# Kernel optimization log

Hardware: AMD Instinct MI355X
Metric: run time of the kernel (lower is better)

## Reference

```python
import jax, jax.numpy as jnp
import numpy as np
import math

B, IMG, P, C_IN = 32, 32, 2, 4
D, TED, L, H = 768, 256, 12, 12
GRID = IMG // P            # 16
N = GRID * GRID            # 256 patches
HD = D // H                # 64 head dim
MLP_H = 4 * D
RPD = 2 * GRID - 1         # 31 relative-position table side


def _ln(x, w, b, eps=1e-6):
    m = x.mean(-1, keepdims=True)
    v = ((x - m) ** 2).mean(-1, keepdims=True)
    return (x - m) * jax.lax.rsqrt(v + eps) * w + b


def _rel_idx():
    c = jnp.arange(GRID)
    ch, cw = jnp.meshgrid(c, c, indexing='ij')
    cf = jnp.stack([ch.reshape(-1), cw.reshape(-1)])          # [2, N]
    rel = cf[:, :, None] - cf[:, None, :] + (GRID - 1)        # [2, N, N] in [0, 2*GRID-2]
    return rel[0], rel[1]


def setup_inputs() -> dict:
    key = jax.random.key(0)
    ks = iter(jax.random.split(key, 64))
    def nrm(shape, s=0.02):
        return jax.random.normal(next(ks), shape, jnp.float32) * s
    z = lambda *s: jnp.zeros(s, jnp.float32)
    o = lambda *s: jnp.ones(s, jnp.float32)
    return dict(
        x=jax.random.normal(next(ks), (B, C_IN, IMG, IMG), jnp.float32),
        t=jax.random.uniform(next(ks), (B,), jnp.float32) * 1000.0,
        patch_w=nrm((D, C_IN, P, P), 0.5), patch_b=z(D),
        pos_embed=nrm((1, N, D)),
        t_w1=nrm((TED, D)), t_b1=z(D), t_w2=nrm((D, D)), t_b2=z(D),
        norm1_w=o(L, D), norm1_b=z(L, D),
        wqs=nrm((L, D, D)), bqs=z(L, D), wqt=nrm((L, D, D)), bqt=z(L, D),
        wks=nrm((L, D, D)), bks=z(L, D), wkt=nrm((L, D, D)), bkt=z(L, D),
        wvs=nrm((L, D, D)), bvs=z(L, D), wvt=nrm((L, D, D)), bvt=z(L, D),
        attn_proj_w=nrm((L, D, D)), attn_proj_b=z(L, D),
        rpb=nrm((L, RPD, RPD, H)),
        norm2_w=o(L, D), norm2_b=z(L, D),
        mlp_w1=nrm((L, D, MLP_H)), mlp_b1=z(L, MLP_H),
        mlp_w2=nrm((L, MLP_H, D)), mlp_b2=z(L, D),
        norm_w=o(D), norm_b=z(D),
        dec_w=nrm((D, P * P * C_IN)), dec_b=z(P * P * C_IN),
    )


def reference(x, t, patch_w, patch_b, pos_embed, t_w1, t_b1, t_w2, t_b2,
              norm1_w, norm1_b, wqs, bqs, wqt, bqt, wks, bks, wkt, bkt,
              wvs, bvs, wvt, bvt, attn_proj_w, attn_proj_b, rpb,
              norm2_w, norm2_b, mlp_w1, mlp_b1, mlp_w2, mlp_b2,
              norm_w, norm_b, dec_w, dec_b):
    Bn = x.shape[0]
    # patch embed: stride==kernel Conv2d as reshape + einsum -> [B, N, D]
    xr = x.reshape(Bn, C_IN, GRID, P, GRID, P)
    x_s = jnp.einsum('bcipjq,ecpq->bije', xr, patch_w).reshape(Bn, N, D) + patch_b
    x_s = x_s + pos_embed
    # sinusoidal time embedding + MLP -> [B, D]
    half = TED // 2
    freq = jnp.exp(jnp.arange(half, dtype=jnp.float32) * (-math.log(10000.0) / (half - 1)))
    emb = t[:, None] * freq[None, :]
    emb = jnp.concatenate([jnp.sin(emb), jnp.cos(emb)], axis=-1)
    x_t = jax.nn.silu(emb @ t_w1 + t_b1) @ t_w2 + t_b2
    ih, iw = _rel_idx()
    scale = HD ** -0.5
    for l in range(L):
        h = _ln(x_s, norm1_w[l], norm1_b[l])
        q = h @ wqs[l] + bqs[l] + (x_t @ wqt[l] + bqt[l])[:, None, :]
        k = h @ wks[l] + bks[l] + (x_t @ wkt[l] + bkt[l])[:, None, :]
        v = h @ wvs[l] + bvs[l] + (x_t @ wvt[l] + bvt[l])[:, None, :]
        q = q.reshape(Bn, N, H, HD)
        k = k.reshape(Bn, N, H, HD)
        v = v.reshape(Bn, N, H, HD)
        bias = rpb[l][ih, iw]                                  # gather: [N, N, H]
        attn = jnp.einsum('bnhd,bmhd->bhnm', q, k) * scale + bias.transpose(2, 0, 1)[None]
        attn = jax.nn.softmax(attn, axis=-1)
        o_ = jnp.einsum('bhnm,bmhd->bnhd', attn, v).reshape(Bn, N, D)
        x_s = x_s + (o_ @ attn_proj_w[l] + attn_proj_b[l])
        h2 = _ln(x_s, norm2_w[l], norm2_b[l])
        x_s = x_s + (jax.nn.silu(h2 @ mlp_w1[l] + mlp_b1[l]) @ mlp_w2[l] + mlp_b2[l])
    x_s = _ln(x_s, norm_w, norm_b)
    x_s = x_s @ dec_w + dec_b                                  # [B, N, P*P*C]
    # unpatchify -> [B, C, IMG, IMG]
    xo = x_s.reshape(Bn, GRID, GRID, C_IN, P, P).transpose(0, 3, 1, 4, 2, 5)
    return xo.reshape(Bn, C_IN, GRID * P, GRID * P)
```

## Files before the change

### kernel.cpp

```cpp
#include <hip/hip_runtime.h>
#include <hip/hip_bf16.h>

typedef __attribute__((ext_vector_type(8))) short short8;
typedef __attribute__((ext_vector_type(4))) short s16x4;
typedef __attribute__((ext_vector_type(4))) float f32x4;
typedef __hip_bfloat16 bf16;

#define AS1 __attribute__((address_space(1)))
#define AS3 __attribute__((address_space(3)))

__device__ __forceinline__ float b2f(short u) {
  union { unsigned int i; float f; } x;
  x.i = ((unsigned int)(unsigned short)u) << 16;
  return x.f;
}
__device__ __forceinline__ short f2bs(float f) {
  bf16 t = __float2bfloat16(f);
  return *reinterpret_cast<short*>(&t);
}

__device__ __forceinline__ void gld_lds16(const void* g, void* lds) {
  __builtin_amdgcn_global_load_lds((const AS1 unsigned int*)g,
                                   (AS3 unsigned int*)lds, 16, 0, 0);
}

__global__ void transpose_conv(const float* __restrict__ src, bf16* __restrict__ dst,
                               int R, int C, int row_off, long long layer_stride) {
  __shared__ float t[32][33];
  int l = blockIdx.z;
  int r0 = blockIdx.y * 32;
  int c0 = blockIdx.x * 32;
  int tx = threadIdx.x & 31, ty = threadIdx.x >> 5;
  const float* s = src + (size_t)l * R * C;
#pragma unroll
  for (int i = 0; i < 4; ++i)
    t[ty + i * 8][tx] = s[(size_t)(r0 + ty + i * 8) * C + c0 + tx];
  __syncthreads();
  bf16* d = dst + (size_t)l * layer_stride;
#pragma unroll
  for (int i = 0; i < 4; ++i) {
    int n = c0 + ty + i * 8, k = r0 + tx;
    d[(size_t)(row_off + n) * R + k] = __float2bfloat16(t[tx][ty + i * 8]);
  }
}

__global__ void dec_transpose(const float* __restrict__ dw, bf16* __restrict__ dwT) {
  int idx = blockIdx.x * 256 + threadIdx.x;
  if (idx >= 12288) return;
  int k = idx % 768, j = idx / 768;
  dwT[j * 768 + k] = __float2bfloat16(dw[k * 16 + j]);
}

__global__ void patch_embed(const float* __restrict__ x, const float* __restrict__ pw,
                            const float* __restrict__ pb, const float* __restrict__ pos,
                            float* __restrict__ xs) {
  int idx = blockIdx.x * 256 + threadIdx.x;
  int d = idx % 768;
  int n = (idx / 768) & 255;
  int b = idx / (768 * 256);
  int gi = n >> 4, gj = n & 15;
  float acc = pb[d];
#pragma unroll
  for (int c = 0; c < 4; ++c)
#pragma unroll
    for (int p = 0; p < 2; ++p)
#pragma unroll
      for (int q = 0; q < 2; ++q)
        acc += x[((b * 4 + c) * 32 + gi * 2 + p) * 32 + gj * 2 + q] *
               pw[((d * 4 + c) * 2 + p) * 2 + q];
  xs[idx] = acc + pos[n * 768 + d];
}

__global__ void temb_kernel(const float* __restrict__ t, float* __restrict__ emb) {
  int b = blockIdx.x;
  int i = threadIdx.x;
  float f = __expf((float)i * (-logf(10000.f) / 127.f));
  float e = t[b] * f;
  emb[b * 256 + i] = sinf(e);
  emb[b * 256 + 128 + i] = cosf(e);
}

template <int MODE>
__global__ void smallmm_red(const float* __restrict__ in, const float* __restrict__ w,
                            const float* __restrict__ bias, void* __restrict__ out, int K) {
  int tid = threadIdx.x;
  int s = tid & 7, o = blockIdx.x * 32 + (tid >> 3);
  int d = o % 768, b = o / 768;
  int Ks = K >> 3, k0 = s * Ks;
  const float* ir = in + b * K + k0;
  const float* wr = w + (size_t)k0 * 768 + d;
  float a = 0.f;
  for (int i = 0; i < Ks; ++i) a += ir[i] * wr[(size_t)i * 768];
  a += __shfl_xor(a, 1);
  a += __shfl_xor(a, 2);
  a += __shfl_xor(a, 4);
  if (s == 0) {
    a += bias[d];
    if (MODE == 0) {
      a = a / (1.f + __expf(-a));
      ((float*)out)[o] = a;
    } else {
      ((bf16*)out)[o] = __float2bfloat16(a);
    }
  }
}

__global__ void build_btab_frag(const float* __restrict__ rpb, bf16* __restrict__ btf) {
  int idx = blockIdx.x * 256 + threadIdx.x;
  int t = idx & 65535;
  int lh = idx >> 16;
  int h = lh % 12, l = lh / 12;
  int r = t & 3; t >>= 2;
  int lane = t & 63; t >>= 6;
  int i = t & 3; t >>= 2;
  int w = t & 3; t >>= 2;
  int jb = t & 1; t >>= 1;
  int hc = t & 7;
  int q = w * 64 + i * 16 + (lane & 15);
  int k = hc * 32 + jb * 16 + (lane >> 4) * 4 + r;
  int ih = (q >> 4) - (k >> 4) + 15;
  int iw = (q & 15) - (k & 15) + 15;
  btf[idx] = __float2bfloat16(8.0f * rpb[((l * 31 + ih) * 31 + iw) * 12 + h]);
}

__global__ __launch_bounds__(256) void ln_bf16_kernel(const float* __restrict__ x,
                                                      const float* __restrict__ w,
                                                      const float* __restrict__ b,
                                                      bf16* __restrict__ out) {
  int row = blockIdx.x * 4 + (threadIdx.x >> 6);
  int lane = threadIdx.x & 63;
  const float* xr = x + (size_t)row * 768;
  float v[12];
  float s = 0.f, s2 = 0.f;
#pragma unroll
  for (int k = 0; k < 12; ++k) {
    v[k] = xr[lane + k * 64];
    s += v[k];
    s2 += v[k] * v[k];
  }
#pragma unroll
  for (int off = 32; off; off >>= 1) {
    s += __shfl_xor(s, off);
    s2 += __shfl_xor(s2, off);
  }
  float m = s * (1.f / 768.f);
  float var = s2 * (1.f / 768.f) - m * m;
  float r = rsqrtf(var + 1e-6f);
  bf16* orow = out + (size_t)row * 768;
#pragma unroll
  for (int k = 0; k < 12; ++k) {
    int c = lane + k * 64;
    orow[c] = __float2bfloat16((v[k] - m) * r * w[c] + b[c]);
  }
}

template <int EPI>
__global__ __launch_bounds__(256) void gemm128(
    const bf16* __restrict__ A, int lda, const bf16* __restrict__ BT, int ldb, int K,
    const float* __restrict__ p0, const float* __restrict__ p1,
    const float* __restrict__ p2, const float* __restrict__ p3,
    const float* __restrict__ p4, const float* __restrict__ p5,
    const float* __restrict__ resid, float* __restrict__ outF,
    bf16* __restrict__ outB, int ldc) {
  __shared__ __align__(16) char lds[65536];
  const int tid = threadIdx.x;
  const int wid = tid >> 6, lane = tid & 63;
  const int wr = wid >> 1, wc = wid & 1;
  const int nwg = gridDim.x * gridDim.y;
  const int bid = blockIdx.y * gridDim.x + blockIdx.x;
  const int swzb = (bid & 7) * (nwg >> 3) + (bid >> 3);
  const int m0 = (swzb / gridDim.x) * 128, n0 = (swzb % gridDim.x) * 128;
  const int l16 = lane & 15, lq = lane >> 4;

  f32x4 acc[4][4];
#pragma unroll
  for (int i = 0; i < 4; ++i)
#pragma unroll
    for (int j = 0; j < 4; ++j) acc[i][j] = f32x4{0.f, 0.f, 0.f, 0.f};

  const int arow = tid >> 3;
  const int aslot = (tid & 7) ^ (arow & 7);
  const bf16* gA = A + (size_t)(m0 + arow) * lda + aslot * 8;
  const bf16* gB = BT + (size_t)(n0 + arow) * ldb + aslot * 8;
  const unsigned offw = (unsigned)__builtin_amdgcn_readfirstlane((tid & ~63) * 16);

  const int NT = K >> 6;
  auto stage = [&](int buf, int t) {
    char* p = lds + buf * 32768;
    const int k = t * 64;
#pragma unroll
    for (int it = 0; it < 4; ++it) {
      gld_lds16(gA + (size_t)it * 32 * lda + k, p + it * 4096 + offw);
      gld_lds16(gB + (size_t)it * 32 * ldb + k, p + 16384 + it * 4096 + offw);
    }
  };

  stage(0, 0);
  const unsigned swb = ((unsigned)(l16 & 7)) << 4;
  for (int t = 0; t < NT; ++t) {
    char* cur = lds + (t & 1) * 32768;
    if (t + 1 < NT) {
      stage((t + 1) & 1, t + 1);
      asm volatile("s_waitcnt vmcnt(8)" ::: "memory");
    } else {
      asm volatile("s_waitcnt vmcnt(0)" ::: "memory");
    }
    __builtin_amdgcn_s_barrier();
#pragma unroll
    for (int ks = 0; ks < 2; ++ks) {
      short8 af[4], bfr[4];
      const unsigned ko = ((unsigned)(ks * 64 + lq * 16)) ^ swb;
#pragma unroll
      for (int i = 0; i < 4; ++i) {
        af[i]  = *(const short8*)(cur + (wr * 64 + i * 16 + l16) * 128 + ko);
        bfr[i] = *(const short8*)(cur + 16384 + (wc * 64 + i * 16 + l16) * 128 + ko);
      }
#pragma unroll
      for (int i = 0; i < 4; ++i)
#pragma unroll
        for (int j = 0; j < 4; ++j)
          acc[i][j] = __builtin_amdgcn_mfma_f32_16x16x32_bf16(af[i], bfr[j], acc[i][j], 0, 0, 0);
    }
    __builtin_amdgcn_s_barrier();
  }

#pragma unroll
  for (int i = 0; i < 4; ++i) {
#pragma unroll
    for (int j = 0; j < 4; ++j) {
#pragma unroll
      for (int r = 0; r < 4; ++r) {
        int row = m0 + wr * 64 + i * 16 + lq * 4 + r;
        int col = n0 + wc * 64 + j * 16 + l16;
        float v = acc[i][j][r];
        if constexpr (EPI == 0) {
          int s = col / 768, d = col % 768;
          int b = row >> 8;
          const float* bs = (s == 0) ? p0 : (s == 1) ? p1 : p2;
          const float* ts = (s == 0) ? p3 : (s == 1) ? p4 : p5;
          v += bs[d] + ts[b * 768 + d];
          outB[(size_t)row * ldc + col] = __float2bfloat16(v);
        } else if constexpr (EPI == 1) {
          v += p0[col] + resid[(size_t)row * ldc + col];
          outF[(size_t)row * ldc + col] = v;
        } else if constexpr (EPI == 2) {
          v += p0[col];
          v = v / (1.f + __expf(-v));
          outB[(size_t)row * ldc + col] = __float2bfloat16(v);
        } else if constexpr (EPI == 3) {
          if (row < 32) {
            int l = col / 2304;
            int r2c = col - l * 2304;
            int s = r2c / 768, d = r2c - s * 768;
            const float* bs = (s == 0) ? p0 : (s == 1) ? p1 : p2;
            v += bs[l * 768 + d];
            outF[(size_t)((l * 3 + s) * 32 + row) * 768 + d] = v;
          }
        } else {
          if (col < 16) {
            v += p0[col];
            int b = row >> 8, n = row & 255;
            int gi = n >> 4, gj = n & 15;
            int c = col >> 2, pp = (col >> 1) & 1, qq = col & 1;
            outF[((b * 4 + c) * 32 + gi * 2 + pp) * 32 + gj * 2 + qq] = v;
          }
        }
      }
    }
  }
}

__global__ __launch_bounds__(256) void attn_mfma(const bf16* __restrict__ qkv,
                                                 const bf16* __restrict__ btf,
                                                 bf16* __restrict__ obuf) {
  __shared__ __align__(16) char lds[65536];
  const int tid = threadIdx.x;
  const int wave = tid >> 6, lane = tid & 63;
  const int l16 = lane & 15, lq = lane >> 4;
  const int b = blockIdx.x / 12, h = blockIdx.x % 12;
  const bf16* qb = qkv + (size_t)b * 256 * 2304;

  {
    const short8* vrow = (const short8*)(qb + (size_t)tid * 2304 + 1536 + h * 64);
    short8 vv[8];
#pragma unroll
    for (int c = 0; c < 8; ++c) vv[c] = vrow[c];
#pragma unroll
    for (int c = 0; c < 8; ++c)
#pragma unroll
      for (int e = 0; e < 8; ++e) {
        int d = c * 8 + e;
        unsigned off = (unsigned)(d * 512 + tid * 2) ^ ((unsigned)(d & 7) << 4);
        *(short*)(lds + off) = vv[c][e];
      }
  }
  short8 qf[4][2];
#pragma unroll
  for (int i = 0; i < 4; ++i)
#pragma unroll
    for (int ks = 0; ks < 2; ++ks)
      qf[i][ks] = *(const short8*)(qb + (size_t)(wave * 64 + i * 16 + l16) * 2304 +
                                   h * 64 + ks * 32 + lq * 8);
  __syncthreads();

  f32x4 oacc[4][4];
#pragma unroll
  for (int i = 0; i < 4; ++i)
#pragma unroll
    for (int j = 0; j < 4; ++j) oacc[i][j] = f32x4{0.f, 0.f, 0.f, 0.f};
  float lp[4] = {0.f, 0.f, 0.f, 0.f};
  const bf16* bl = btf + (size_t)h * 65536 + lane * 4;
  const unsigned swzv = ((unsigned)(l16 & 7)) << 4;
  const unsigned swzp = ((unsigned)(l16 & 3)) << 4;

  for (int hc = 0; hc < 8; ++hc) {
    short8 kf[2][2];
#pragma unroll
    for (int jb = 0; jb < 2; ++jb) {
      const bf16* kr = qb + (size_t)(hc * 32 + jb * 16 + l16) * 2304 + 768 + h * 64 + lq * 8;
      kf[jb][0] = *(const short8*)(kr);
      kf[jb][1] = *(const short8*)(kr + 32);
    }
    f32x4 sacc[4][2];
#pragma unroll
    for (int i = 0; i < 4; ++i)
#pragma unroll
      for (int jb = 0; jb < 2; ++jb) {
        s16x4 bv = *(const s16x4*)(bl + ((size_t)((hc * 2 + jb) * 16 + wave * 4 + i) << 8));
        sacc[i][jb] = f32x4{b2f(bv[0]), b2f(bv[1]), b2f(bv[2]), b2f(bv[3])};
      }
#pragma unroll
    for (int jb = 0; jb < 2; ++jb)
#pragma unroll
      for (int i = 0; i < 4; ++i) {
        sacc[i][jb] = __builtin_amdgcn_mfma_f32_16x16x32_bf16(kf[jb][0], qf[i][0], sacc[i][jb], 0, 0, 0);
        sacc[i][jb] = __builtin_amdgcn_mfma_f32_16x16x32_bf16(kf[jb][1], qf[i][1], sacc[i][jb], 0, 0, 0);
      }
    char* Pw = lds + 32768 + (hc & 1) * 16384 + wave * 4096;
#pragma unroll
    for (int i = 0; i < 4; ++i)
#pragma unroll
      for (int jb = 0; jb < 2; ++jb) {
        float p0 = __expf(sacc[i][jb][0] * 0.125f);
        float p1 = __expf(sacc[i][jb][1] * 0.125f);
        float p2 = __expf(sacc[i][jb][2] * 0.125f);
        float p3 = __expf(sacc[i][jb][3] * 0.125f);
        lp[i] += (p0 + p1) + (p2 + p3);
        s16x4 pk = {f2bs(p0), f2bs(p1), f2bs(p2), f2bs(p3)};
        *(s16x4*)(Pw + (i * 16 + l16) * 64 + (((unsigned)(jb * 32 + lq * 8)) ^ swzp)) = pk;
      }
    asm volatile("s_waitcnt lgkmcnt(0)" ::: "memory");
    __builtin_amdgcn_sched_barrier(0);
    short8 pa[4], vb[4];
#pragma unroll
    for (int i = 0; i < 4; ++i)
      pa[i] = *(const short8*)(Pw + (i * 16 + l16) * 64 + (((unsigned)(lq * 16)) ^ swzp));
#pragma unroll
    for (int dj = 0; dj < 4; ++dj)
      vb[dj] = *(const short8*)(lds + (dj * 16 + l16) * 512 +
                                (((unsigned)(hc * 64 + lq * 16)) ^ swzv));
#pragma unroll
    for (int i = 0; i < 4; ++i)
#pragma unroll
      for (int dj = 0; dj < 4; ++dj)
        oacc[i][dj] = __builtin_amdgcn_mfma_f32_16x16x32_bf16(pa[i], vb[dj], oacc[i][dj], 0, 0, 0);
  }

#pragma unroll
  for (int i = 0; i < 4; ++i) {
    float l = lp[i];
    l += __shfl_xor(l, 16);
    l += __shfl_xor(l, 32);
#pragma unroll
    for (int r = 0; r < 4; ++r) {
      float linv = 1.f / __shfl(l, lq * 4 + r);
      int grow = b * 256 + wave * 64 + i * 16 + lq * 4 + r;
#pragma unroll
      for (int dj = 0; dj < 4; ++dj)
        obuf[(size_t)grow * 768 + h * 64 + dj * 16 + l16] =
            __float2bfloat16(oacc[i][dj][r] * linv);
    }
  }
}

extern "C" void kernel_launch(void* const* d_in, const int* in_sizes, int n_in,
                              void* d_out, int out_size, void* d_ws, size_t ws_size,
                              hipStream_t stream) {
  (void)in_sizes; (void)n_in; (void)out_size; (void)ws_size;
  const float* x       = (const float*)d_in[0];
  const float* t_in    = (const float*)d_in[1];
  const float* patch_w = (const float*)d_in[2];
  const float* patch_b = (const float*)d_in[3];
  const float* pos     = (const float*)d_in[4];
  const float* t_w1    = (const float*)d_in[5];
  const float* t_b1    = (const float*)d_in[6];
  const float* t_w2    = (const float*)d_in[7];
  const float* t_b2    = (const float*)d_in[8];
  const float* norm1_w = (const float*)d_in[9];
  const float* norm1_b = (const float*)d_in[10];
  const float* wqs     = (const float*)d_in[11];
  const float* bqs     = (const float*)d_in[12];
  const float* wqt     = (const float*)d_in[13];
  const float* bqt     = (const float*)d_in[14];
  const float* wks     = (const float*)d_in[15];
  const float* bks     = (const float*)d_in[16];
  const float* wkt     = (const float*)d_in[17];
  const float* bkt     = (const float*)d_in[18];
  const float* wvs     = (const float*)d_in[19];
  const float* bvs     = (const float*)d_in[20];
  const float* wvt     = (const float*)d_in[21];
  const float* bvt     = (const float*)d_in[22];
  const float* projw   = (const float*)d_in[23];
  const float* projb   = (const float*)d_in[24];
  const float* rpb     = (const float*)d_in[25];
  const float* norm2_w = (const float*)d_in[26];
  const float* norm2_b = (const float*)d_in[27];
  const float* mlp_w1  = (const float*)d_in[28];
  const float* mlp_b1  = (const float*)d_in[29];
  const float* mlp_w2  = (const float*)d_in[30];
  const float* mlp_b2  = (const float*)d_in[31];
  const float* norm_w  = (const float*)d_in[32];
  const float* norm_b  = (const float*)d_in[33];
  const float* dec_w   = (const float*)d_in[34];
  const float* dec_b   = (const float*)d_in[35];

  char* ws = (char*)d_ws;
  size_t off = 0;
  auto alloc = [&](size_t bytes) -> void* {
    void* p = ws + off;
    off += (bytes + 255) & ~(size_t)255;
    return p;
  };
  bf16* wqkvT = (bf16*)alloc(12ull * 2304 * 768 * 2);
  bf16* projT = (bf16*)alloc(12ull * 768 * 768 * 2);
  bf16* mlp1T = (bf16*)alloc(12ull * 3072 * 768 * 2);
  bf16* mlp2T = (bf16*)alloc(12ull * 768 * 3072 * 2);
  bf16* wtT   = (bf16*)alloc(12ull * 2304 * 768 * 2);
  float* xs   = (float*)alloc(8192ull * 768 * 4);
  bf16* hbuf  = (bf16*)alloc(8192ull * 768 * 2);
  bf16* qkvb  = (bf16*)alloc(8192ull * 2304 * 2);
  bf16* obuf  = (bf16*)alloc(8192ull * 768 * 2);
  bf16* btabf = (bf16*)alloc(12ull * 12 * 256 * 256 * 2);
  float* ttok = (float*)alloc(12ull * 3 * 32 * 768 * 4);
  bf16* xtb   = (bf16*)alloc(128ull * 768 * 2);
  bf16* dwT   = (bf16*)alloc(128ull * 768 * 2);
  float* emb  = (float*)alloc(32ull * 256 * 4);
  float* h1   = (float*)alloc(32ull * 768 * 4);
  bf16* hmlp  = qkvb;

  hipMemsetAsync(xtb, 0, 128ull * 768 * 2, stream);
  hipMemsetAsync(dwT, 0, 128ull * 768 * 2, stream);

  transpose_conv<<<dim3(24, 24, 12), 256, 0, stream>>>(wqs, wqkvT, 768, 768, 0, 2304ll * 768);
  transpose_conv<<<dim3(24, 24, 12), 256, 0, stream>>>(wks, wqkvT, 768, 768, 768, 2304ll * 768);
  transpose_conv<<<dim3(24, 24, 12), 256, 0, stream>>>(wvs, wqkvT, 768, 768, 1536, 2304ll * 768);
  transpose_conv<<<dim3(24, 24, 12), 256, 0, stream>>>(projw, projT, 768, 768, 0, 768ll * 768);
  transpose_conv<<<dim3(96, 24, 12), 256, 0, stream>>>(mlp_w1, mlp1T, 768, 3072, 0, 3072ll * 768);
  transpose_conv<<<dim3(24, 96, 12), 256, 0, stream>>>(mlp_w2, mlp2T, 3072, 768, 0, 768ll * 3072);
  transpose_conv<<<dim3(24, 24, 12), 256, 0, stream>>>(wqt, wtT, 768, 768, 0, 2304ll * 768);
  transpose_conv<<<dim3(24, 24, 12), 256, 0, stream>>>(wkt, wtT, 768, 768, 768, 2304ll * 768);
  transpose_conv<<<dim3(24, 24, 12), 256, 0, stream>>>(wvt, wtT, 768, 768, 1536, 2304ll * 768);
  dec_transpose<<<48, 256, 0, stream>>>(dec_w, dwT);
  build_btab_frag<<<36864, 256, 0, stream>>>(rpb, btabf);

  temb_kernel<<<32, 128, 0, stream>>>(t_in, emb);
  smallmm_red<0><<<768, 256, 0, stream>>>(emb, t_w1, t_b1, h1, 256);
  smallmm_red<1><<<768, 256, 0, stream>>>(h1, t_w2, t_b2, xtb, 768);
  gemm128<3><<<dim3(216, 1), 256, 0, stream>>>(
      xtb, 768, wtT, 768, 768, bqt, bkt, bvt, nullptr, nullptr, nullptr,
      nullptr, ttok, nullptr, 0);

  patch_embed<<<24576, 256, 0, stream>>>(x, patch_w, patch_b, pos, xs);

  for (int l = 0; l < 12; ++l) {
    ln_bf16_kernel<<<2048, 256, 0, stream>>>(xs, norm1_w + l * 768, norm1_b + l * 768, hbuf);
    gemm128<0><<<dim3(18, 64), 256, 0, stream>>>(
        hbuf, 768, wqkvT + (size_t)l * 2304 * 768, 768, 768,
        bqs + l * 768, bks + l * 768, bvs + l * 768,
        ttok + (size_t)(l * 3 + 0) * 32 * 768,
        ttok + (size_t)(l * 3 + 1) * 32 * 768,
        ttok + (size_t)(l * 3 + 2) * 32 * 768,
        nullptr, nullptr, qkvb, 2304);
    attn_mfma<<<384, 256, 0, stream>>>(qkvb, btabf + (size_t)l * 12 * 65536, obuf);
    gemm128<1><<<dim3(6, 64), 256, 0, stream>>>(
        obuf, 768, projT + (size_t)l * 768 * 768, 768, 768,
        projb + l * 768, nullptr, nullptr, nullptr, nullptr, nullptr,
        xs, xs, nullptr, 768);
    ln_bf16_kernel<<<2048, 256, 0, stream>>>(xs, norm2_w + l * 768, norm2_b + l * 768, hbuf);
    gemm128<2><<<dim3(24, 64), 256, 0, stream>>>(
        hbuf, 768, mlp1T + (size_t)l * 3072 * 768, 768, 768,
        mlp_b1 + l * 3072, nullptr, nullptr, nullptr, nullptr, nullptr,
        nullptr, nullptr, hmlp, 3072);
    gemm128<1><<<dim3(6, 64), 256, 0, stream>>>(
        hmlp, 3072, mlp2T + (size_t)l * 768 * 3072, 3072, 3072,
        mlp_b2 + l * 768, nullptr, nullptr, nullptr, nullptr, nullptr,
        xs, xs, nullptr, 768);
  }
  ln_bf16_kernel<<<2048, 256, 0, stream>>>(xs, norm_w, norm_b, hbuf);
  gemm128<4><<<dim3(1, 64), 256, 0, stream>>>(
      hbuf, 768, dwT, 768, 768, dec_b, nullptr, nullptr, nullptr, nullptr, nullptr,
      nullptr, (float*)d_out, nullptr, 0);
}
```

Measured before the change: 2.772 ms.

## Shrink attention LDS, add MFMA priority hints, restructure patch embedding per patch

The attention kernel drops the double-buffered P scratch region, shrinking LDS from 64KB to 48KB so more blocks can be resident per CU. It also raises wave priority around the MFMA sections with s_setprio. Separately, patch_embed now runs one block per patch, staging the 16 input pixels in shared memory and reusing them across three output channels per thread. A single P buffer is safe because each wave waits on its own LDS ops before reading it back, but this removes the slack between iterations.

```diff
diff --git a/kernel.cpp b/kernel.cpp
--- a/kernel.cpp
+++ b/kernel.cpp
@@ -51,24 +51,33 @@
   dwT[j * 768 + k] = __float2bfloat16(dw[k * 16 + j]);
 }
 
-__global__ void patch_embed(const float* __restrict__ x, const float* __restrict__ pw,
-                            const float* __restrict__ pb, const float* __restrict__ pos,
-                            float* __restrict__ xs) {
-  int idx = blockIdx.x * 256 + threadIdx.x;
-  int d = idx % 768;
-  int n = (idx / 768) & 255;
-  int b = idx / (768 * 256);
+__global__ __launch_bounds__(256) void patch_embed(const float* __restrict__ x,
+                                                   const float* __restrict__ pw,
+                                                   const float* __restrict__ pb,
+                                                   const float* __restrict__ pos,
+                                                   float* __restrict__ xs) {
+  __shared__ float xp[16];
+  int bn = blockIdx.x;
+  int n = bn & 255, b = bn >> 8;
   int gi = n >> 4, gj = n & 15;
-  float acc = pb[d];
-#pragma unroll
-  for (int c = 0; c < 4; ++c)
-#pragma unroll
-    for (int p = 0; p < 2; ++p)
-#pragma unroll
-      for (int q = 0; q < 2; ++q)
-        acc += x[((b * 4 + c) * 32 + gi * 2 + p) * 32 + gj * 2 + q] *
-               pw[((d * 4 + c) * 2 + p) * 2 + q];
-  xs[idx] = acc + pos[n * 768 + d];
+  int tid = threadIdx.x;
+  if (tid < 16) {
+    int c = tid >> 2, p = (tid >> 1) & 1, q = tid & 1;
+    xp[tid] = x[((b * 4 + c) * 32 + gi * 2 + p) * 32 + gj * 2 + q];
+  }
+  __syncthreads();
+  float xv[16];
+#pragma unroll
+  for (int j = 0; j < 16; ++j) xv[j] = xp[j];
+#pragma unroll
+  for (int it = 0; it < 3; ++it) {
+    int d = tid + it * 256;
+    const float* pwr = pw + d * 16;
+    float acc = pb[d];
+#pragma unroll
+    for (int j = 0; j < 16; ++j) acc += xv[j] * pwr[j];
+    xs[(size_t)bn * 768 + d] = acc + pos[n * 768 + d];
+  }
 }
 
 __global__ void temb_kernel(const float* __restrict__ t, float* __restrict__ emb) {
@@ -273,7 +282,7 @@
 __global__ __launch_bounds__(256) void attn_mfma(const bf16* __restrict__ qkv,
                                                  const bf16* __restrict__ btf,
                                                  bf16* __restrict__ obuf) {
-  __shared__ __align__(16) char lds[65536];
+  __shared__ __align__(16) char lds[49152];
   const int tid = threadIdx.x;
   const int wave = tid >> 6, lane = tid & 63;
   const int l16 = lane & 15, lq = lane >> 4;
@@ -312,6 +321,7 @@
   const bf16* bl = btf + (size_t)h * 65536 + lane * 4;
   const unsigned swzv = ((unsigned)(l16 & 7)) << 4;
   const unsigned swzp = ((unsigned)(l16 & 3)) << 4;
+  char* Pw = lds + 32768 + wave * 4096;
 
   for (int hc = 0; hc < 8; ++hc) {
     short8 kf[2][2];
@@ -329,6 +339,7 @@
         s16x4 bv = *(const s16x4*)(bl + ((size_t)((hc * 2 + jb) * 16 + wave * 4 + i) << 8));
         sacc[i][jb] = f32x4{b2f(bv[0]), b2f(bv[1]), b2f(bv[2]), b2f(bv[3])};
       }
+    __builtin_amdgcn_s_setprio(1);
 #pragma unroll
     for (int jb = 0; jb < 2; ++jb)
 #pragma unroll
@@ -336,7 +347,7 @@
         sacc[i][jb] = __builtin_amdgcn_mfma_f32_16x16x32_bf16(kf[jb][0], qf[i][0], sacc[i][jb], 0, 0, 0);
         sacc[i][jb] = __builtin_amdgcn_mfma_f32_16x16x32_bf16(kf[jb][1], qf[i][1], sacc[i][jb], 0, 0, 0);
       }
-    char* Pw = lds + 32768 + (hc & 1) * 16384 + wave * 4096;
+    __builtin_amdgcn_s_setprio(0);
 #pragma unroll
     for (int i = 0; i < 4; ++i)
 #pragma unroll
@@ -359,11 +370,13 @@
     for (int dj = 0; dj < 4; ++dj)
       vb[dj] = *(const short8*)(lds + (dj * 16 + l16) * 512 +
                                 (((unsigned)(hc * 64 + lq * 16)) ^ swzv));
+    __builtin_amdgcn_s_setprio(1);
 #pragma unroll
     for (int i = 0; i < 4; ++i)
 #pragma unroll
       for (int dj = 0; dj < 4; ++dj)
         oacc[i][dj] = __builtin_amdgcn_mfma_f32_16x16x32_bf16(pa[i], vb[dj], oacc[i][dj], 0, 0, 0);
+    __builtin_amdgcn_s_setprio(0);
   }
 
 #pragma unroll
@@ -470,7 +483,7 @@
       xtb, 768, wtT, 768, 768, bqt, bkt, bvt, nullptr, nullptr, nullptr,
       nullptr, ttok, nullptr, 0);
 
-  patch_embed<<<24576, 256, 0, stream>>>(x, patch_w, patch_b, pos, xs);
+  patch_embed<<<8192, 256, 0, stream>>>(x, patch_w, patch_b, pos, xs);
 
   for (int l = 0; l < 12; ++l) {
     ln_bf16_kernel<<<2048, 256, 0, stream>>>(xs, norm1_w + l * 768, norm1_b + l * 768, hbuf);
```

Result: no change. 2.749 ms (-0.8%).
